# Performance work log

Measured on AMD Instinct MI355X. Metric: run time of the kernel, lower is better.

The kernel has to match this reference:

```python
import jax, jax.numpy as jnp
import numpy as np

N, D = 4096, 1024

def setup_inputs() -> dict:
    key = jax.random.key(0)
    ks = jax.random.split(key, 7)
    s = 1.0 / np.sqrt(D)
    return {
        "x": jax.random.normal(ks[0], (N, D), dtype=jnp.float32),
        "Wq": jax.random.uniform(ks[1], (D, D), jnp.float32, -s, s),
        "bq": jax.random.uniform(ks[2], (D,), jnp.float32, -s, s),
        "Wk": jax.random.uniform(ks[3], (D, D), jnp.float32, -s, s),
        "bk": jax.random.uniform(ks[4], (D,), jnp.float32, -s, s),
        "Wv": jax.random.uniform(ks[5], (D, D), jnp.float32, -s, s),
        "bv": jax.random.uniform(ks[6], (D,), jnp.float32, -s, s),
    }

def reference(x, Wq, bq, Wk, bk, Wv, bv):
    # Linear layers: y = x @ W^T + b (torch convention, W is [out, in]; here square)
    Q = x @ Wq.T + bq  # [N, D]
    K = x @ Wk.T + bk  # [N, D]
    V = x @ Wv.T + bv  # [N, D]
    scores = (Q @ K.T) / jnp.sqrt(jnp.asarray(x.shape[-1], x.dtype))  # [N, N]
    attn = jax.nn.softmax(scores, axis=-1)
    return attn @ V  # [N, D]
```

## Files before the change

kernel.cpp:

```cpp
#include <hip/hip_runtime.h>


#define N_TOK 4096
#define DDIM  1024

typedef short s16x4 __attribute__((ext_vector_type(4)));
typedef short s16x8 __attribute__((ext_vector_type(8)));
typedef float f32x4 __attribute__((ext_vector_type(4)));

#define VMCNT0() asm volatile("s_waitcnt vmcnt(0)" ::: "memory")
#define VMCNT4() asm volatile("s_waitcnt vmcnt(4)" ::: "memory")
#define VMCNT6() asm volatile("s_waitcnt vmcnt(6)" ::: "memory")
#define VMCNT8() asm volatile("s_waitcnt vmcnt(8)" ::: "memory")
#define LGKMCNT0() asm volatile("s_waitcnt lgkmcnt(0)" ::: "memory")
#define SCHEDB() __builtin_amdgcn_sched_barrier(0)
#define BARRIER() do { asm volatile("" ::: "memory"); \
                       __builtin_amdgcn_s_barrier();  \
                       asm volatile("" ::: "memory"); } while (0)

__device__ inline short f2b(float f) {
  unsigned int u = __float_as_uint(f);
  unsigned int r = (u + 0x7FFFu + ((u >> 16) & 1u)) >> 16;
  return (short)(unsigned short)r;
}

__device__ __forceinline__ void gld_lds16(const short* g, short* l) {
  __builtin_amdgcn_global_load_lds(
      (const __attribute__((address_space(1))) unsigned int*)g,
      (__attribute__((address_space(3))) unsigned int*)l, 16, 0, 0);
}

__device__ __forceinline__ void xcd_remap(int gx, int& bx, int& by) {
  const int L = by * gx + bx;
  const int g = L & 7, h = L >> 3;
  by = g * 4 + (h & 3);
  bx = h >> 2;
}
__device__ __forceinline__ void xcd_remap16(int gx, int& bx, int& by) {
  const int L = by * gx + bx;
  const int g = L & 7, h = L >> 3;
  by = g * 2 + (h & 1);
  bx = h >> 1;
}

template<int MODE>
__device__ __forceinline__ void gemm_pipe128(
    const short* __restrict__ A, const short* __restrict__ B,
    void* __restrict__ C, const float* __restrict__ aux,
    short (*smem)[(128 + 128) * 64],
    int K, int ld, int ldc, float scale, int row0, int col0)
{
  constexpr int BM = 128, BN = 128, BK = 64;
  const int NT = K / BK;

  const int tid  = threadIdx.x;
  const int wave = tid >> 6, lane = tid & 63;
  const int wm = wave >> 1, wn = wave & 1;
  const int quad = lane >> 4, lr = lane & 15;

  auto stage = [&](int t, int sl) {
    #pragma unroll
    for (int c = 0; c < 8; c++) {
      const int id = c * 256 + tid;
      const int r  = id >> 3;
      const int q  = (id & 7) ^ (r & 7);
      const short* src = (r < BM)
          ? A + (size_t)(row0 + r) * ld + t * BK + q * 8
          : B + (size_t)(col0 + r - BM) * ld + t * BK + q * 8;
      gld_lds16(src, &smem[sl][(c * 256 + wave * 64) * 8]);
    }
  };

  f32x4 acc[4][4];
  #pragma unroll
  for (int i = 0; i < 4; i++)
    #pragma unroll
    for (int j = 0; j < 4; j++) acc[i][j] = {0.f, 0.f, 0.f, 0.f};

  stage(0, 0);
  stage(1, 1);
  VMCNT8();
  BARRIER();

  for (int t = 0; t < NT; t++) {
    const int sl = t & 1;
    const short* As = smem[sl];
    const short* Bs = smem[sl] + BM * BK;

    s16x8 af[2][4], bf[2][4];
    #pragma unroll
    for (int h = 0; h < 2; h++) {
      #pragma unroll
      for (int i = 0; i < 4; i++) {
        const int row = wm * 64 + i * 16 + lr;
        const int ch = (h * 4 + quad) ^ (row & 7);
        af[h][i] = *reinterpret_cast<const s16x8*>(&As[(row * 8 + ch) * 8]);
      }
      #pragma unroll
      for (int j = 0; j < 4; j++) {
        const int row = wn * 64 + j * 16 + lr;
        const int ch = (h * 4 + quad) ^ (row & 7);
        bf[h][j] = *reinterpret_cast<const s16x8*>(&Bs[(row * 8 + ch) * 8]);
      }
    }
    LGKMCNT0();
    SCHEDB();
    BARRIER();

    const bool pf = (t + 2) < NT;
    if (pf) stage(t + 2, sl);

    __builtin_amdgcn_s_setprio(1);
    #pragma unroll
    for (int h = 0; h < 2; h++)
      #pragma unroll
      for (int i = 0; i < 4; i++)
        #pragma unroll
        for (int j = 0; j < 4; j++)
          acc[i][j] = __builtin_amdgcn_mfma_f32_16x16x32_bf16(
              af[h][i], bf[h][j], acc[i][j], 0, 0, 0);
    __builtin_amdgcn_s_setprio(0);

    if (pf) { VMCNT8(); } else { VMCNT0(); }
    BARRIER();
  }

  if constexpr (MODE == 0) {
    float bb[4];
    #pragma unroll
    for (int j = 0; j < 4; j++) bb[j] = aux[col0 + wn * 64 + j * 16 + lr];
    #pragma unroll
    for (int i = 0; i < 4; i++) {
      const int r0 = row0 + wm * 64 + i * 16 + quad * 4;
      #pragma unroll
      for (int j = 0; j < 4; j++) {
        const int c = col0 + wn * 64 + j * 16 + lr;
        #pragma unroll
        for (int r = 0; r < 4; r++)
          ((short*)C)[(size_t)(r0 + r) * ldc + c] = f2b(acc[i][j][r] * scale + bb[j]);
      }
    }
  } else {
    float bb[4];
    #pragma unroll
    for (int j = 0; j < 4; j++) bb[j] = aux[col0 + wn * 64 + j * 16 + lr];
    short* trans = &smem[0][0];
    #pragma unroll
    for (int i = 0; i < 4; i++) {
      const int rl = wm * 64 + i * 16 + quad * 4;
      #pragma unroll
      for (int j = 0; j < 4; j++) {
        const int cl = wn * 64 + j * 16 + lr;
        s16x4 v;
        #pragma unroll
        for (int r = 0; r < 4; r++) v[r] = f2b(acc[i][j][r] * scale + bb[j]);
        *reinterpret_cast<s16x4*>(&trans[cl * 136 + rl]) = v;
      }
    }
    BARRIER();
    #pragma unroll
    for (int s = 0; s < 8; s++) {
      const int u = s * 256 + tid;
      const int cc = u >> 4;
      const int seg = u & 15;
      s16x8 v = *reinterpret_cast<const s16x8*>(&trans[cc * 136 + seg * 8]);
      *reinterpret_cast<s16x8*>(
          &((short*)C)[(size_t)(col0 + cc) * ldc + row0 + seg * 8]) = v;
    }
  }
}

#define XU  (N_TOK * DDIM / 8)
#define WU  (DDIM * DDIM / 8)
#define NCVT ((XU + 3 * WU) / 256)
__global__ __launch_bounds__(256)
void cvt_all(const float* __restrict__ x,  const float* __restrict__ wq,
             const float* __restrict__ wk, const float* __restrict__ wv,
             short* __restrict__ xb, short* __restrict__ wqb,
             short* __restrict__ wkb, short* __restrict__ wvb,
             float* __restrict__ rowsum)
{
  if (blockIdx.x >= NCVT) {
    float4 z = {0.f, 0.f, 0.f, 0.f};
    float4* p = reinterpret_cast<float4*>(rowsum) + threadIdx.x * 4;
    p[0] = z; p[1] = z; p[2] = z; p[3] = z;
    return;
  }
  int gid = blockIdx.x * 256 + threadIdx.x;
  const float* src; short* dst; int off;
  if (gid < XU)               { src = x;  dst = xb;  off = gid; }
  else if (gid < XU + WU)     { src = wq; dst = wqb; off = gid - XU; }
  else if (gid < XU + 2 * WU) { src = wk; dst = wkb; off = gid - XU - WU; }
  else                        { src = wv; dst = wvb; off = gid - XU - 2 * WU; }
  const float4* g = reinterpret_cast<const float4*>(src) + (size_t)off * 2;
  float4 a = g[0], b = g[1];
  s16x8 o;
  o[0] = f2b(a.x); o[1] = f2b(a.y); o[2] = f2b(a.z); o[3] = f2b(a.w);
  o[4] = f2b(b.x); o[5] = f2b(b.y); o[6] = f2b(b.z); o[7] = f2b(b.w);
  reinterpret_cast<s16x8*>(dst)[off] = o;
}

__global__ __launch_bounds__(256, 2)
void k_qkv(const short* __restrict__ xb,
           const short* __restrict__ Wqb, const short* __restrict__ Wkb,
           const short* __restrict__ Wvb,
           const float* __restrict__ bq, const float* __restrict__ bk,
           const float* __restrict__ bv,
           short* __restrict__ Qb, short* __restrict__ Kb, short* __restrict__ Vt)
{
  __shared__ short smem[2][(128 + 128) * 64];
  int bx = blockIdx.x, by = blockIdx.y;
  xcd_remap(DDIM / 128, bx, by);
  if (blockIdx.z == 0) {
    gemm_pipe128<0>(xb, Wqb, Qb, bq, smem, DDIM, DDIM, DDIM,
                    1.0f, by * 128, bx * 128);
  } else if (blockIdx.z == 1) {
    gemm_pipe128<0>(xb, Wkb, Kb, bk, smem, DDIM, DDIM, DDIM,
                    1.0f, by * 128, bx * 128);
  } else {
    gemm_pipe128<3>(xb, Wvb, Vt, bv, smem, DDIM, DDIM, N_TOK,
                    1.0f, by * 128, bx * 128);
  }
}

#define READ_AF(As, MH) do {                                                  \
    _Pragma("unroll")                                                         \
    for (int kh = 0; kh < 2; kh++)                                            \
      _Pragma("unroll")                                                       \
      for (int f = 0; f < 4; f++) {                                           \
        const int row_ = wm * 128 + (MH) * 64 + f * 16 + lr;                  \
        const int ch_ = (kh * 4 + quad) ^ (row_ & 7);                         \
        af[kh][f] = *reinterpret_cast<const s16x8*>(&(As)[(row_ * 8 + ch_) * 8]); \
      }                                                                       \
  } while (0)

#define READ_BF(Bs, NH, BF) do {                                              \
    _Pragma("unroll")                                                         \
    for (int kh = 0; kh < 2; kh++)                                            \
      _Pragma("unroll")                                                       \
      for (int g = 0; g < 2; g++) {                                           \
        const int row_ = wn * 64 + (NH) * 32 + g * 16 + lr;                   \
        const int ch_ = (kh * 4 + quad) ^ (row_ & 7);                         \
        BF[kh][g] = *reinterpret_cast<const s16x8*>(&(Bs)[(row_ * 8 + ch_) * 8]); \
      }                                                                       \
  } while (0)

#define MFMA_Q(MH, NH, BF) do {                                               \
    __builtin_amdgcn_s_setprio(1);                                            \
    _Pragma("unroll")                                                         \
    for (int kh = 0; kh < 2; kh++)                                            \
      _Pragma("unroll")                                                       \
      for (int f = 0; f < 4; f++)                                             \
        _Pragma("unroll")                                                     \
        for (int g = 0; g < 2; g++)                                           \
          acc[(MH) * 4 + f][(NH) * 2 + g] =                                   \
              __builtin_amdgcn_mfma_f32_16x16x32_bf16(                        \
                  af[kh][f], BF[kh][g], acc[(MH) * 4 + f][(NH) * 2 + g],      \
                  0, 0, 0);                                                   \
    __builtin_amdgcn_s_setprio(0);                                            \
  } while (0)

__global__ __launch_bounds__(512, 2)
void k_score(const short* __restrict__ Qb, const short* __restrict__ Kb,
             short* __restrict__ SP, float* __restrict__ rowsum)
{
  constexpr int NITER = 8;
  __shared__ short smem[2][32768];

  int bx = blockIdx.x, by = blockIdx.y;
  xcd_remap16(16, bx, by);
  const int row0 = by * 256, col0 = bx * 256;

  const int tid  = threadIdx.x;
  const int wave = tid >> 6, lane = tid & 63;
  const int wm = wave >> 2, wn = wave & 3;
  const int quad = lane >> 4, lr = lane & 15;

  auto stage_h = [&](int t, int b, int h) {
    const short* gbase = (h < 2)
        ? Qb + (size_t)(row0 + (h & 1) * 128) * DDIM
        : Kb + (size_t)(col0 + (h & 1) * 128) * DDIM;
    short* dst = &smem[b][(h >> 1) * 16384 + (h & 1) * 8192];
    #pragma unroll
    for (int c = 0; c < 2; c++) {
      const int id = c * 512 + tid;
      const int r  = id >> 3;
      const int q  = (id & 7) ^ (r & 7);
      gld_lds16(gbase + (size_t)r * DDIM + t * 64 + q * 8,
                dst + (c * 512 + wave * 64) * 8);
    }
  };

  s16x8 af[2][4], bf0[2][2], bf1[2][2];
  f32x4 acc[8][4];
  #pragma unroll
  for (int i = 0; i < 8; i++)
    #pragma unroll
    for (int j = 0; j < 4; j++) acc[i][j] = {0.f, 0.f, 0.f, 0.f};

  const short* As0 = smem[0];
  const short* Bs0 = smem[0] + 16384;
  const short* As1 = smem[1];
  const short* Bs1 = smem[1] + 16384;

  stage_h(0, 0, 2); stage_h(0, 0, 3); stage_h(0, 0, 0); stage_h(0, 0, 1);
  stage_h(1, 1, 2); stage_h(1, 1, 0);
  VMCNT4();
  BARRIER();

  for (int i = 0; i < NITER; i++) {
    const int t1 = 2 * i + 1;
    const bool more = (i + 1) < NITER;

    READ_AF(As0, 0); READ_BF(Bs0, 0, bf0);
    stage_h(t1, 1, 3);
    BARRIER(); LGKMCNT0(); SCHEDB();
    MFMA_Q(0, 0, bf0);
    BARRIER();
    READ_BF(Bs0, 1, bf1);
    stage_h(t1, 1, 1);
    BARRIER(); LGKMCNT0(); SCHEDB();
    MFMA_Q(0, 1, bf1);
    BARRIER();
    READ_AF(As0, 1);
    if (more) stage_h(t1 + 1, 0, 2);
    BARRIER(); LGKMCNT0(); SCHEDB();
    MFMA_Q(1, 1, bf1);
    BARRIER();
    if (more) { stage_h(t1 + 1, 0, 0); VMCNT4(); } else { VMCNT0(); }
    BARRIER();
    MFMA_Q(1, 0, bf0);
    BARRIER();
    READ_AF(As1, 0); READ_BF(Bs1, 0, bf0);
    if (more) stage_h(t1 + 1, 0, 3);
    BARRIER(); LGKMCNT0(); SCHEDB();
    MFMA_Q(0, 0, bf0);
    BARRIER();
    READ_BF(Bs1, 1, bf1);
    if (more) stage_h(t1 + 1, 0, 1);
    BARRIER(); LGKMCNT0(); SCHEDB();
    MFMA_Q(0, 1, bf1);
    BARRIER();
    READ_AF(As1, 1);
    if (more) stage_h(t1 + 2, 1, 2);
    BARRIER(); LGKMCNT0(); SCHEDB();
    MFMA_Q(1, 1, bf1);
    BARRIER();
    if (more) { stage_h(t1 + 2, 1, 0); VMCNT4(); } else { VMCNT0(); }
    BARRIER();
    MFMA_Q(1, 0, bf0);
    BARRIER();
  }

  constexpr float scale = 0.03125f;
  #pragma unroll
  for (int i = 0; i < 8; i++) {
    const int r0 = row0 + wm * 128 + i * 16 + quad * 4;
    float ex[4][4];
    #pragma unroll
    for (int j = 0; j < 4; j++) {
      const int c = col0 + wn * 64 + j * 16 + lr;
      #pragma unroll
      for (int r = 0; r < 4; r++) {
        ex[j][r] = __expf(acc[i][j][r] * scale);
        SP[(size_t)(r0 + r) * N_TOK + c] = f2b(ex[j][r]);
      }
    }
    #pragma unroll
    for (int r = 0; r < 4; r++) {
      float s = 0.f;
      #pragma unroll
      for (int j = 0; j < 4; j++) s += ex[j][r];
      s += __shfl_xor(s, 1, 64);
      s += __shfl_xor(s, 2, 64);
      s += __shfl_xor(s, 4, 64);
      s += __shfl_xor(s, 8, 64);
      if (lr == 0) atomicAdd(&rowsum[r0 + r], s);
    }
  }
}

__global__ __launch_bounds__(256, 2)
void k_pv(const short* __restrict__ SP, const short* __restrict__ Vt,
          float* __restrict__ out, const float* __restrict__ rowsum)
{
  constexpr int BM = 128, BN = 64, BK = 64;
  constexpr int NT = N_TOK / BK;
  __shared__ short smem[2][(BM + BN) * BK];

  int bx = blockIdx.x, by = blockIdx.y;
  xcd_remap(DDIM / 64, bx, by);
  const int row0 = by * BM, col0 = bx * BN;

  const int tid  = threadIdx.x;
  const int wave = tid >> 6, lane = tid & 63;
  const int wm = wave >> 1, wn = wave & 1;
  const int quad = lane >> 4, lr = lane & 15;

  auto stage = [&](int t, int sl) {
    #pragma unroll
    for (int c = 0; c < 6; c++) {
      const int id = c * 256 + tid;
      const int r  = id >> 3;
      const int q  = (id & 7) ^ (r & 7);
      const short* src = (r < BM)
          ? SP + (size_t)(row0 + r) * N_TOK + t * BK + q * 8
          : Vt + (size_t)(col0 + r - BM) * N_TOK + t * BK + q * 8;
      gld_lds16(src, &smem[sl][(c * 256 + wave * 64) * 8]);
    }
  };

  f32x4 acc[4][2];
  #pragma unroll
  for (int i = 0; i < 4; i++)
    #pragma unroll
    for (int j = 0; j < 2; j++) acc[i][j] = {0.f, 0.f, 0.f, 0.f};

  stage(0, 0);
  stage(1, 1);
  VMCNT6();
  BARRIER();

  for (int t = 0; t < NT; t++) {
    const int sl = t & 1;
    const short* As = smem[sl];
    const short* Bs = smem[sl] + BM * BK;

    s16x8 af[2][4], bf[2][2];
    #pragma unroll
    for (int h = 0; h < 2; h++) {
      #pragma unroll
      for (int i = 0; i < 4; i++) {
        const int row = wm * 64 + i * 16 + lr;
        const int ch = (h * 4 + quad) ^ (row & 7);
        af[h][i] = *reinterpret_cast<const s16x8*>(&As[(row * 8 + ch) * 8]);
      }
      #pragma unroll
      for (int j = 0; j < 2; j++) {
        const int row = wn * 32 + j * 16 + lr;
        const int ch = (h * 4 + quad) ^ (row & 7);
        bf[h][j] = *reinterpret_cast<const s16x8*>(&Bs[(row * 8 + ch) * 8]);
      }
    }
    LGKMCNT0();
    SCHEDB();
    BARRIER();

    const bool pf = (t + 2) < NT;
    if (pf) stage(t + 2, sl);

    __builtin_amdgcn_s_setprio(1);
    #pragma unroll
    for (int h = 0; h < 2; h++)
      #pragma unroll
      for (int i = 0; i < 4; i++)
        #pragma unroll
        for (int j = 0; j < 2; j++)
          acc[i][j] = __builtin_amdgcn_mfma_f32_16x16x32_bf16(
              af[h][i], bf[h][j], acc[i][j], 0, 0, 0);
    __builtin_amdgcn_s_setprio(0);

    if (pf) { VMCNT6(); } else { VMCNT0(); }
    BARRIER();
  }

  #pragma unroll
  for (int i = 0; i < 4; i++) {
    const int r0 = row0 + wm * 64 + i * 16 + quad * 4;
    float linv[4];
    #pragma unroll
    for (int r = 0; r < 4; r++) linv[r] = 1.0f / rowsum[r0 + r];
    #pragma unroll
    for (int j = 0; j < 2; j++) {
      const int c = col0 + wn * 32 + j * 16 + lr;
      #pragma unroll
      for (int r = 0; r < 4; r++)
        out[(size_t)(r0 + r) * DDIM + c] = acc[i][j][r] * linv[r];
    }
  }
}

extern "C" void kernel_launch(void* const* d_in, const int* in_sizes, int n_in,
                              void* d_out, int out_size, void* d_ws, size_t ws_size,
                              hipStream_t stream)
{
  const float* x  = (const float*)d_in[0];
  const float* Wq = (const float*)d_in[1];
  const float* bq = (const float*)d_in[2];
  const float* Wk = (const float*)d_in[3];
  const float* bk = (const float*)d_in[4];
  const float* Wv = (const float*)d_in[5];
  const float* bv = (const float*)d_in[6];
  float* out = (float*)d_out;

  char* ws = (char*)d_ws;
  const size_t MB = 1024 * 1024;
  short* Qb  = (short*)(ws + 0 * MB);
  short* Kb  = (short*)(ws + 8 * MB);
  short* Vt  = (short*)(ws + 24 * MB);
  short* SP  = (short*)(ws + 32 * MB);
  short* xb  = (short*)(ws + 32 * MB);
  short* Wqb = (short*)(ws + 40 * MB);
  short* Wkb = (short*)(ws + 42 * MB);
  short* Wvb = (short*)(ws + 44 * MB);
  float* rowsum = (float*)(ws + 64 * MB);

  dim3 b256(256);

  cvt_all<<<dim3(NCVT + 1), b256, 0, stream>>>(
      x, Wq, Wk, Wv, xb, Wqb, Wkb, Wvb, rowsum);

  k_qkv<<<dim3(DDIM / 128, N_TOK / 128, 3), b256, 0, stream>>>(
      xb, Wqb, Wkb, Wvb, bq, bk, bv, Qb, Kb, Vt);

  k_score<<<dim3(16, 16), dim3(512), 0, stream>>>(Qb, Kb, SP, rowsum);

  k_pv<<<dim3(DDIM / 64, N_TOK / 128), b256, 0, stream>>>(
      SP, Vt, out, rowsum);
}
```

Before: 196.8 us.

## Fuse Q, K, V projections into one kernel sharing the x tile

The three separate QKV GEMM blocks (grid z=3) are merged into one block that computes Q, K and V for the same 128x128 output tile. Each x tile is loaded once into LDS and reused against three weight tiles, with BK reduced to 32 to fit four tiles in LDS. This cuts redundant x loads and triples MFMA work per LDS A-fragment, but it needs 3x the accumulator registers (48 f32x4 per thread), launches a third as many blocks, and doubles the number of K iterations and barriers.

```diff
diff --git a/kernel.cpp b/kernel.cpp
--- a/kernel.cpp
+++ b/kernel.cpp
@@ -41,133 +41,6 @@
   const int g = L & 7, h = L >> 3;
   by = g * 2 + (h & 1);
   bx = h >> 1;
-}
-
-template<int MODE>
-__device__ __forceinline__ void gemm_pipe128(
-    const short* __restrict__ A, const short* __restrict__ B,
-    void* __restrict__ C, const float* __restrict__ aux,
-    short (*smem)[(128 + 128) * 64],
-    int K, int ld, int ldc, float scale, int row0, int col0)
-{
-  constexpr int BM = 128, BN = 128, BK = 64;
-  const int NT = K / BK;
-
-  const int tid  = threadIdx.x;
-  const int wave = tid >> 6, lane = tid & 63;
-  const int wm = wave >> 1, wn = wave & 1;
-  const int quad = lane >> 4, lr = lane & 15;
-
-  auto stage = [&](int t, int sl) {
-    #pragma unroll
-    for (int c = 0; c < 8; c++) {
-      const int id = c * 256 + tid;
-      const int r  = id >> 3;
-      const int q  = (id & 7) ^ (r & 7);
-      const short* src = (r < BM)
-          ? A + (size_t)(row0 + r) * ld + t * BK + q * 8
-          : B + (size_t)(col0 + r - BM) * ld + t * BK + q * 8;
-      gld_lds16(src, &smem[sl][(c * 256 + wave * 64) * 8]);
-    }
-  };
-
-  f32x4 acc[4][4];
-  #pragma unroll
-  for (int i = 0; i < 4; i++)
-    #pragma unroll
-    for (int j = 0; j < 4; j++) acc[i][j] = {0.f, 0.f, 0.f, 0.f};
-
-  stage(0, 0);
-  stage(1, 1);
-  VMCNT8();
-  BARRIER();
-
-  for (int t = 0; t < NT; t++) {
-    const int sl = t & 1;
-    const short* As = smem[sl];
-    const short* Bs = smem[sl] + BM * BK;
-
-    s16x8 af[2][4], bf[2][4];
-    #pragma unroll
-    for (int h = 0; h < 2; h++) {
-      #pragma unroll
-      for (int i = 0; i < 4; i++) {
-        const int row = wm * 64 + i * 16 + lr;
-        const int ch = (h * 4 + quad) ^ (row & 7);
-        af[h][i] = *reinterpret_cast<const s16x8*>(&As[(row * 8 + ch) * 8]);
-      }
-      #pragma unroll
-      for (int j = 0; j < 4; j++) {
-        const int row = wn * 64 + j * 16 + lr;
-        const int ch = (h * 4 + quad) ^ (row & 7);
-        bf[h][j] = *reinterpret_cast<const s16x8*>(&Bs[(row * 8 + ch) * 8]);
-      }
-    }
-    LGKMCNT0();
-    SCHEDB();
-    BARRIER();
-
-    const bool pf = (t + 2) < NT;
-    if (pf) stage(t + 2, sl);
-
-    __builtin_amdgcn_s_setprio(1);
-    #pragma unroll
-    for (int h = 0; h < 2; h++)
-      #pragma unroll
-      for (int i = 0; i < 4; i++)
-        #pragma unroll
-        for (int j = 0; j < 4; j++)
-          acc[i][j] = __builtin_amdgcn_mfma_f32_16x16x32_bf16(
-              af[h][i], bf[h][j], acc[i][j], 0, 0, 0);
-    __builtin_amdgcn_s_setprio(0);
-
-    if (pf) { VMCNT8(); } else { VMCNT0(); }
-    BARRIER();
-  }
-
-  if constexpr (MODE == 0) {
-    float bb[4];
-    #pragma unroll
-    for (int j = 0; j < 4; j++) bb[j] = aux[col0 + wn * 64 + j * 16 + lr];
-    #pragma unroll
-    for (int i = 0; i < 4; i++) {
-      const int r0 = row0 + wm * 64 + i * 16 + quad * 4;
-      #pragma unroll
-      for (int j = 0; j < 4; j++) {
-        const int c = col0 + wn * 64 + j * 16 + lr;
-        #pragma unroll
-        for (int r = 0; r < 4; r++)
-          ((short*)C)[(size_t)(r0 + r) * ldc + c] = f2b(acc[i][j][r] * scale + bb[j]);
-      }
-    }
-  } else {
-    float bb[4];
-    #pragma unroll
-    for (int j = 0; j < 4; j++) bb[j] = aux[col0 + wn * 64 + j * 16 + lr];
-    short* trans = &smem[0][0];
-    #pragma unroll
-    for (int i = 0; i < 4; i++) {
-      const int rl = wm * 64 + i * 16 + quad * 4;
-      #pragma unroll
-      for (int j = 0; j < 4; j++) {
-        const int cl = wn * 64 + j * 16 + lr;
-        s16x4 v;
-        #pragma unroll
-        for (int r = 0; r < 4; r++) v[r] = f2b(acc[i][j][r] * scale + bb[j]);
-        *reinterpret_cast<s16x4*>(&trans[cl * 136 + rl]) = v;
-      }
-    }
-    BARRIER();
-    #pragma unroll
-    for (int s = 0; s < 8; s++) {
-      const int u = s * 256 + tid;
-      const int cc = u >> 4;
-      const int seg = u & 15;
-      s16x8 v = *reinterpret_cast<const s16x8*>(&trans[cc * 136 + seg * 8]);
-      *reinterpret_cast<s16x8*>(
-          &((short*)C)[(size_t)(col0 + cc) * ldc + row0 + seg * 8]) = v;
-    }
-  }
 }
 
 #define XU  (N_TOK * DDIM / 8)
@@ -208,18 +81,143 @@
            const float* __restrict__ bv,
            short* __restrict__ Qb, short* __restrict__ Kb, short* __restrict__ Vt)
 {
-  __shared__ short smem[2][(128 + 128) * 64];
+  constexpr int BK = 32;
+  constexpr int NT = DDIM / BK;
+  __shared__ short smem[2][4 * 128 * BK];
+
   int bx = blockIdx.x, by = blockIdx.y;
-  xcd_remap(DDIM / 128, bx, by);
-  if (blockIdx.z == 0) {
-    gemm_pipe128<0>(xb, Wqb, Qb, bq, smem, DDIM, DDIM, DDIM,
-                    1.0f, by * 128, bx * 128);
-  } else if (blockIdx.z == 1) {
-    gemm_pipe128<0>(xb, Wkb, Kb, bk, smem, DDIM, DDIM, DDIM,
-                    1.0f, by * 128, bx * 128);
-  } else {
-    gemm_pipe128<3>(xb, Wvb, Vt, bv, smem, DDIM, DDIM, N_TOK,
-                    1.0f, by * 128, bx * 128);
+  xcd_remap(8, bx, by);
+  const int row0 = by * 128, col0 = bx * 128;
+
+  const int tid  = threadIdx.x;
+  const int wave = tid >> 6, lane = tid & 63;
+  const int wm = wave >> 1, wn = wave & 1;
+  const int quad = lane >> 4, lr = lane & 15;
+
+  auto stage = [&](int t, int sl) {
+    #pragma unroll
+    for (int c = 0; c < 8; c++) {
+      const int id = c * 256 + tid;
+      const int r  = id >> 2;
+      const int q  = (id & 3) ^ (r & 3) ^ ((r >> 2) & 3);
+      const int rr = r & 127;
+      const short* src =
+          (r < 128) ? xb  + (size_t)(row0 + rr) * DDIM + t * BK + q * 8 :
+          (r < 256) ? Wqb + (size_t)(col0 + rr) * DDIM + t * BK + q * 8 :
+          (r < 384) ? Wkb + (size_t)(col0 + rr) * DDIM + t * BK + q * 8 :
+                      Wvb + (size_t)(col0 + rr) * DDIM + t * BK + q * 8;
+      gld_lds16(src, &smem[sl][(c * 256 + wave * 64) * 8]);
+    }
+  };
+
+  f32x4 aq[4][4], ak[4][4], av[4][4];
+  #pragma unroll
+  for (int i = 0; i < 4; i++)
+    #pragma unroll
+    for (int j = 0; j < 4; j++) {
+      aq[i][j] = {0.f, 0.f, 0.f, 0.f};
+      ak[i][j] = {0.f, 0.f, 0.f, 0.f};
+      av[i][j] = {0.f, 0.f, 0.f, 0.f};
+    }
+
+  stage(0, 0);
+  stage(1, 1);
+  VMCNT8();
+  BARRIER();
+
+  for (int t = 0; t < NT; t++) {
+    const int sl = t & 1;
+    const short* As = smem[sl];
+    const short* Bq = smem[sl] + 4096;
+    const short* Bk = smem[sl] + 8192;
+    const short* Bv = smem[sl] + 12288;
+
+    s16x8 af[4], fq[4], fk[4], fv[4];
+    #pragma unroll
+    for (int i = 0; i < 4; i++) {
+      const int row = wm * 64 + i * 16 + lr;
+      const int ch = quad ^ (row & 3) ^ ((row >> 2) & 3);
+      af[i] = *reinterpret_cast<const s16x8*>(&As[(row * 4 + ch) * 8]);
+    }
+    #pragma unroll
+    for (int j = 0; j < 4; j++) {
+      const int row = wn * 64 + j * 16 + lr;
+      const int ch = quad ^ (row & 3) ^ ((row >> 2) & 3);
+      fq[j] = *reinterpret_cast<const s16x8*>(&Bq[(row * 4 + ch) * 8]);
+      fk[j] = *reinterpret_cast<const s16x8*>(&Bk[(row * 4 + ch) * 8]);
+      fv[j] = *reinterpret_cast<const s16x8*>(&Bv[(row * 4 + ch) * 8]);
+    }
+    LGKMCNT0();
+    SCHEDB();
+    BARRIER();
+
+    const bool pf = (t + 2) < NT;
+    if (pf) stage(t + 2, sl);
+
+    __builtin_amdgcn_s_setprio(1);
+    #pragma unroll
+    for (int i = 0; i < 4; i++)
+      #pragma unroll
+      for (int j = 0; j < 4; j++) {
+        aq[i][j] = __builtin_amdgcn_mfma_f32_16x16x32_bf16(af[i], fq[j], aq[i][j], 0, 0, 0);
+        ak[i][j] = __builtin_amdgcn_mfma_f32_16x16x32_bf16(af[i], fk[j], ak[i][j], 0, 0, 0);
+        av[i][j] = __builtin_amdgcn_mfma_f32_16x16x32_bf16(af[i], fv[j], av[i][j], 0, 0, 0);
+      }
+    __builtin_amdgcn_s_setprio(0);
+
+    if (pf) { VMCNT8(); } else { VMCNT0(); }
+    BARRIER();
+  }
+
+  {
+    float bbq[4], bbk[4];
+    #pragma unroll
+    for (int j = 0; j < 4; j++) {
+      bbq[j] = bq[col0 + wn * 64 + j * 16 + lr];
+      bbk[j] = bk[col0 + wn * 64 + j * 16 + lr];
+    }
+    #pragma unroll
+    for (int i = 0; i < 4; i++) {
+      const int r0 = row0 + wm * 64 + i * 16 + quad * 4;
+      #pragma unroll
+      for (int j = 0; j < 4; j++) {
+        const int c = col0 + wn * 64 + j * 16 + lr;
+        #pragma unroll
+        for (int r = 0; r < 4; r++) {
+          Qb[(size_t)(r0 + r) * DDIM + c] = f2b(aq[i][j][r] + bbq[j]);
+          Kb[(size_t)(r0 + r) * DDIM + c] = f2b(ak[i][j][r] + bbk[j]);
+        }
+      }
+    }
+  }
+
+  {
+    float bbv[4];
+    #pragma unroll
+    for (int j = 0; j < 4; j++) bbv[j] = bv[col0 + wn * 64 + j * 16 + lr];
+    short* trans = &smem[0][0];
+    #pragma unroll
+    for (int i = 0; i < 4; i++) {
+      const int rl = wm * 64 + i * 16 + quad * 4;
+      #pragma unroll
+      for (int j = 0; j < 4; j++) {
+        const int cl = wn * 64 + j * 16 + lr;
+        s16x4 v;
+        #pragma unroll
+        for (int r = 0; r < 4; r++) v[r] = f2b(av[i][j][r] + bbv[j]);
+        *reinterpret_cast<s16x4*>(&trans[cl * 136 + rl]) = v;
+      }
+    }
+    BARRIER();
+    #pragma unroll
+    for (int s = 0; s < 8; s++) {
+      const int u = s * 256 + tid;
+      const int cc = u >> 4;
+      const int seg = u & 15;
+      s16x8 v = *reinterpret_cast<const s16x8*>(&trans[cc * 136 + seg * 8]);
+      *reinterpret_cast<s16x8*>(
+          &Vt[(size_t)(col0 + cc) * N_TOK + row0 + seg * 8]) = v;
+    }
   }
 }
 
@@ -510,7 +508,7 @@
   cvt_all<<<dim3(NCVT + 1), b256, 0, stream>>>(
       x, Wq, Wk, Wv, xb, Wqb, Wkb, Wvb, rowsum);
 
-  k_qkv<<<dim3(DDIM / 128, N_TOK / 128, 3), b256, 0, stream>>>(
+  k_qkv<<<dim3(8, 32), b256, 0, stream>>>(
       xb, Wqb, Wkb, Wvb, bq, bk, bv, Qb, Kb, Vt);
 
   k_score<<<dim3(16, 16), dim3(512), 0, stream>>>(Qb, Kb, SP, rowsum);
```

After: 272.0 us. +38.2%, slower.
